# Performance work log

Measured on AMD Instinct MI355X. Metric: run time of the kernel, lower is better.

The kernel has to match this reference:

```python
import jax, jax.numpy as jnp
import numpy as np

N, E, F_IN, HID, OUT, HEADS, HC, L, EV, ED = 50000, 800000, 128, 96, 64, 8, 12, 6, 1000, 32
ACT_SLOPE = 0.01   # LeakyReLU default (act_layer)
ATT_SLOPE = 0.2    # GATv2 attention leaky relu
EPS = 1e-5         # GraphNorm eps


def setup_inputs() -> dict:
    key = jax.random.key(0)
    ks = jax.random.split(key, 16)
    r = lambda k, shp, s=0.05: jax.random.normal(k, shp, jnp.float32) * s
    z = lambda shp: jnp.zeros(shp, jnp.float32)
    o = lambda shp: jnp.ones(shp, jnp.float32)
    return {
        "x": jax.random.normal(ks[0], (N, F_IN), jnp.float32),
        "edge_index": jax.random.randint(ks[1], (2, E), 0, N),
        "edge_weight": jax.random.uniform(ks[2], (E,), jnp.float32),
        "edge_code": jax.random.randint(ks[3], (E,), 0, EV),
        "edge_emb": r(ks[4], (EV, ED), 0.1),
        "lin_in_W": r(ks[5], (F_IN, HID)), "lin_in_b": z((HID,)),
        "gn0_w": o((HID,)), "gn0_b": z((HID,)), "gn0_ms": o((HID,)),
        "Wl": r(ks[6], (L, HID, HID)), "bl": z((L, HID)),
        "Wr": r(ks[7], (L, HID, HID)), "br": z((L, HID)),
        "We": r(ks[8], (L, ED, HID)),
        "att": r(ks[9], (L, HEADS, HC)),
        "gbias": z((L, HID)),
        "gn_w": o((L, HID)), "gn_b": z((L, HID)), "gn_ms": o((L, HID)),
        "lin_out_W": r(ks[10], (HID, OUT)), "lin_out_b": z((OUT,)),
    }


def graph_norm(x, w, b, ms):
    # PyG GraphNorm on a single graph: mean over nodes, learnable mean scale
    mean = x.mean(axis=0, keepdims=True)
    out = x - ms * mean
    var = (out * out).mean(axis=0, keepdims=True)
    return w * out * jax.lax.rsqrt(var + EPS) + b


def gatv2_conv(h, src, dst, ew, ea, Wl_, bl_, Wr_, br_, We_, att_, bias_):
    # GATv2 with edge features; messages weighted by edge_weight (WGATv2Conv)
    xl = (h @ Wl_ + bl_).reshape(N, HEADS, HC)  # source transform
    xr = (h @ Wr_ + br_).reshape(N, HEADS, HC)  # target transform
    ee = (ea @ We_).reshape(E, HEADS, HC)       # edge transform
    s = jax.nn.leaky_relu(xl[src] + xr[dst] + ee, ATT_SLOPE)  # [E,H,C]
    logits = jnp.einsum('ehc,hc->eh', s, att_)  # [E,H]
    # numerically stable segment softmax over incoming edges of each dst node
    m = jax.ops.segment_max(logits, dst, num_segments=N)
    m = jnp.where(jnp.isfinite(m), m, 0.0)      # isolated nodes -> -inf max
    p = jnp.exp(logits - m[dst])
    zsum = jax.ops.segment_sum(p, dst, num_segments=N)
    alpha = p / (zsum[dst] + 1e-16)             # [E,H]
    msg = xl[src] * (alpha * ew[:, None])[..., None]  # [E,H,C]
    out = jax.ops.segment_sum(msg, dst, num_segments=N)  # [N,H,C]
    return out.reshape(N, HID) + bias_


def reference(x, edge_index, edge_weight, edge_code, edge_emb,
              lin_in_W, lin_in_b, gn0_w, gn0_b, gn0_ms,
              Wl, bl, Wr, br, We, att, gbias,
              gn_w, gn_b, gn_ms, lin_out_W, lin_out_b):
    src, dst = edge_index[0], edge_index[1]
    ea = edge_emb[edge_code]                    # [E,ED]
    h = graph_norm(x @ lin_in_W + lin_in_b, gn0_w, gn0_b, gn0_ms)
    for l in range(L):  # DeepGCNLayer 'res+': norm -> act -> conv, + residual
        t = graph_norm(h, gn_w[l], gn_b[l], gn_ms[l])
        t = jax.nn.leaky_relu(t, ACT_SLOPE)
        t = gatv2_conv(t, src, dst, edge_weight, ea,
                       Wl[l], bl[l], Wr[l], br[l], We[l], att[l], gbias[l])
        h = h + t
    return h @ lin_out_W + lin_out_b
```

## Files before the change

kernel.cpp:

```cpp
#include <hip/hip_runtime.h>
#include <hip/hip_bf16.h>

constexpr int NN   = 50000;
constexpr int NE   = 800000;
constexpr int FIN  = 128;
constexpr int HIDC = 96;
constexpr int FOUT = 64;
constexpr int NHEAD= 8;
constexpr int HCH  = 12;
constexpr int NLAY = 6;
constexpr int EVOC = 1000;
constexpr int EDIM = 32;
constexpr float ACT_SLOPE = 0.01f;
constexpr float ATT_SLOPE = 0.2f;
constexpr float GN_EPS = 1e-5f;
constexpr int GN_BLOCKS = 256;
constexpr int NSCB = (NN + 255)/256;

typedef __hip_bfloat16 bf16;
typedef __attribute__((ext_vector_type(8))) short bf16x8;
typedef __attribute__((ext_vector_type(4))) float f32x4;

__device__ __forceinline__ float bfu(unsigned u, int hi){
    return __uint_as_float(hi ? (u & 0xffff0000u) : (u << 16));
}

__global__ void k_hist(const int* __restrict__ dst, int* __restrict__ deg){
    int e = blockIdx.x*blockDim.x + threadIdx.x;
    if(e < NE) atomicAdd(&deg[dst[e]], 1);
}

__global__ __launch_bounds__(256) void k_scan1(const int* __restrict__ deg,
        int* __restrict__ pre, int* __restrict__ bsum){
    __shared__ int s[256];
    int tid = threadIdx.x;
    int idx = blockIdx.x*256 + tid;
    int v = (idx < NN) ? deg[idx] : 0;
    s[tid] = v; __syncthreads();
    #pragma unroll
    for(int off=1; off<256; off<<=1){
        int t = (tid>=off) ? s[tid-off] : 0;
        __syncthreads();
        s[tid] += t;
        __syncthreads();
    }
    if(idx < NN) pre[idx] = s[tid] - v;
    if(tid == 255) bsum[blockIdx.x] = s[255];
}

__global__ __launch_bounds__(256) void k_scan2(const int* __restrict__ bsum,
        int* __restrict__ boffs){
    __shared__ int s[256];
    int tid = threadIdx.x;
    int v = (tid < NSCB) ? bsum[tid] : 0;
    s[tid] = v; __syncthreads();
    #pragma unroll
    for(int off=1; off<256; off<<=1){
        int t = (tid>=off) ? s[tid-off] : 0;
        __syncthreads();
        s[tid] += t;
        __syncthreads();
    }
    if(tid < NSCB) boffs[tid] = s[tid] - v;
}

__global__ __launch_bounds__(256) void k_scan3(const int* __restrict__ pre,
        const int* __restrict__ boffs, int* __restrict__ rowptr, int* __restrict__ cursor){
    int tid = threadIdx.x;
    int idx = blockIdx.x*256 + tid;
    if(idx < NN){
        rowptr[idx] = pre[idx] + boffs[blockIdx.x];
        cursor[idx] = 0;
    }
    if(blockIdx.x == 0 && tid == 0) rowptr[NN] = NE;
}

__global__ void k_scatter(const int* __restrict__ src, const int* __restrict__ dst,
                          const int* __restrict__ code, const float* __restrict__ ew,
                          const int* __restrict__ rowptr, int* __restrict__ cursor,
                          int4* __restrict__ epk){
    int e = blockIdx.x*blockDim.x + threadIdx.x;
    if(e >= NE) return;
    int d = dst[e];
    int pos = rowptr[d] + atomicAdd(&cursor[d], 1);
    epk[pos] = make_int4(src[e], code[e], __float_as_int(ew[e]), 0);
}

__global__ __launch_bounds__(256) void k_trall(const float* __restrict__ Wl,
        const float* __restrict__ Wr, const float* __restrict__ Win, const float* __restrict__ Wout,
        bf16* __restrict__ wlt, bf16* __restrict__ wrt, bf16* __restrict__ wint, bf16* __restrict__ wot){
    int seg = blockIdx.y;
    const float* W; bf16* Wt; int K, N;
    if(seg < 6)      { W = Wl  + seg*9216;     Wt = wlt + seg*9216;     K = 96;  N = 96; }
    else if(seg < 12){ W = Wr  + (seg-6)*9216; Wt = wrt + (seg-6)*9216; K = 96;  N = 96; }
    else if(seg==12) { W = Win;                Wt = wint;               K = 128; N = 96; }
    else             { W = Wout;               Wt = wot;                K = 96;  N = 64; }
    int i = blockIdx.x*256 + threadIdx.x;
    if(i >= K*N) return;
    int k = i / N, nn = i - k*N;
    Wt[(size_t)nn*K + k] = __float2bfloat16(W[i]);
}

template<int K, int NC, typename OT>
__global__ __launch_bounds__(256) void k_gemm(const float* __restrict__ A,
        const float* __restrict__ W, const float* __restrict__ bias,
        OT* __restrict__ C, int M, int wstride, int cstride){
    constexpr int CPT = NC/16;
    W += (size_t)blockIdx.y * wstride;
    C += (size_t)blockIdx.y * cstride;
    __shared__ float At[K][68];
    int tid = threadIdx.x;
    int m0 = blockIdx.x*64;
    for(int i=tid; i<64*K; i+=256){
        int r = i / K, k = i - r*K;
        int row = m0 + r;
        At[k][r] = (row < M) ? A[(size_t)row*K + k] : 0.f;
    }
    __syncthreads();
    int tr = tid>>4, tc = tid&15;
    const float* wr = W + tc*CPT;
    float acc[4][CPT];
    #pragma unroll
    for(int i=0;i<4;i++)
        #pragma unroll
        for(int j=0;j<CPT;j++) acc[i][j]=0.f;
    #pragma unroll 4
    for(int k=0;k<K;k++){
        float a[4], w[CPT];
        #pragma unroll
        for(int i=0;i<4;i++) a[i] = At[k][tr*4+i];
        #pragma unroll
        for(int j=0;j<CPT;j++) w[j] = wr[k*NC + j];
        #pragma unroll
        for(int i=0;i<4;i++)
            #pragma unroll
            for(int j=0;j<CPT;j++) acc[i][j] += a[i]*w[j];
    }
    #pragma unroll
    for(int i=0;i<4;i++){
        int row = m0 + tr*4 + i;
        if(row < M){
            OT* cp = C + (size_t)row*NC + tc*CPT;
            #pragma unroll
            for(int j=0;j<CPT;j++){
                float v = acc[i][j] + (bias ? bias[tc*CPT+j] : 0.f);
                if constexpr (sizeof(OT)==2) cp[j] = __float2bfloat16(v);
                else cp[j] = v;
            }
        }
    }
}

template<int K, int NC, bool GN, bool DUAL, typename OT>
__global__ __launch_bounds__(256) void k_mfgemm(const float* __restrict__ A,
        const bf16* __restrict__ W1t, const float* __restrict__ b1,
        const bf16* __restrict__ W2t, const float* __restrict__ b2,
        const float* __restrict__ gscale, const float* __restrict__ gshift, float slope,
        OT* __restrict__ C1, OT* __restrict__ C2, int M){
    constexpr int KP = K + 8;
    constexpr int F4R = K/4;
    constexpr int NF4 = 64*F4R;
    constexpr int KS = K/32;
    constexpr int NT = NC/16;
    __shared__ bf16 At[64][KP];
    int tid = threadIdx.x;
    int m0 = blockIdx.x*64;
    for(int idx = tid; idx < NF4; idx += 256){
        int r = idx / F4R, c4 = idx - r*F4R;
        int row = m0 + r;
        float4 v = (row < M) ? ((const float4*)A)[(size_t)row*F4R + c4]
                             : make_float4(0.f,0.f,0.f,0.f);
        float vv[4] = {v.x, v.y, v.z, v.w};
        bf16* dp = &At[r][c4*4];
        #pragma unroll
        for(int c=0;c<4;c++){
            float u = vv[c];
            if constexpr (GN){
                int k = c4*4 + c;
                u = gscale[k]*u + gshift[k];
                u = (u > 0.f) ? u : slope*u;
            }
            dp[c] = __float2bfloat16(u);
        }
    }
    __syncthreads();
    int w = tid >> 6, l = tid & 63;
    int mrow = l & 15;
    int kg = (l >> 4) * 8;
    f32x4 acc1[NT], acc2[NT];
    #pragma unroll
    for(int nt=0; nt<NT; nt++){
        acc1[nt] = (f32x4){0.f,0.f,0.f,0.f};
        if constexpr (DUAL) acc2[nt] = (f32x4){0.f,0.f,0.f,0.f};
    }
    const bf16* a_base = &At[w*16 + mrow][0];
    #pragma unroll
    for(int ks=0; ks<KS; ks++){
        bf16x8 a = *(const bf16x8*)(a_base + ks*32 + kg);
        #pragma unroll
        for(int nt=0; nt<NT; nt++){
            int n = nt*16 + mrow;
            bf16x8 bfr = *(const bf16x8*)(W1t + (size_t)n*K + ks*32 + kg);
            acc1[nt] = __builtin_amdgcn_mfma_f32_16x16x32_bf16(a, bfr, acc1[nt], 0,0,0);
            if constexpr (DUAL){
                bf16x8 bfr2 = *(const bf16x8*)(W2t + (size_t)n*K + ks*32 + kg);
                acc2[nt] = __builtin_amdgcn_mfma_f32_16x16x32_bf16(a, bfr2, acc2[nt], 0,0,0);
            }
        }
    }
    int rbase = m0 + w*16 + (l>>4)*4;
    #pragma unroll
    for(int nt=0; nt<NT; nt++){
        int n = nt*16 + mrow;
        float bb1 = b1[n];
        float bb2 = 0.f;
        if constexpr (DUAL) bb2 = b2[n];
        #pragma unroll
        for(int r=0;r<4;r++){
            int row = rbase + r;
            if(row < M){
                float v1 = acc1[nt][r] + bb1;
                if constexpr (sizeof(OT)==2) C1[(size_t)row*NC + n] = __float2bfloat16(v1);
                else                         C1[(size_t)row*NC + n] = v1;
                if constexpr (DUAL){
                    float v2 = acc2[nt][r] + bb2;
                    C2[(size_t)row*NC + n] = __float2bfloat16(v2);
                }
            }
        }
    }
}

__global__ __launch_bounds__(384) void k_gn_reduce(const float* __restrict__ x, float* __restrict__ partial){
    int tid = threadIdx.x;
    const float4* x4 = (const float4*)x;
    constexpr int TOT4 = NN*HIDC/4;
    const int stride = GN_BLOCKS*384;
    float s0=0,s1=0,s2=0,s3=0, q0=0,q1=0,q2=0,q3=0;
    for(int i = blockIdx.x*384 + tid; i < TOT4; i += stride){
        float4 v = x4[i];
        s0+=v.x; q0+=v.x*v.x;
        s1+=v.y; q1+=v.y*v.y;
        s2+=v.z; q2+=v.z*v.z;
        s3+=v.w; q3+=v.w*v.w;
    }
    __shared__ float ls[384][4], lq[384][4];
    ls[tid][0]=s0; ls[tid][1]=s1; ls[tid][2]=s2; ls[tid][3]=s3;
    lq[tid][0]=q0; lq[tid][1]=q1; lq[tid][2]=q2; lq[tid][3]=q3;
    __syncthreads();
    if(tid < 96){
        int g = tid >> 2, c = tid & 3;
        float a=0.f, b=0.f;
        #pragma unroll
        for(int j=0;j<16;j++){
            a += ls[g + 24*j][c];
            b += lq[g + 24*j][c];
        }
        partial[blockIdx.x*192 + g*4 + c]      = a;
        partial[blockIdx.x*192 + 96 + g*4 + c] = b;
    }
}

__global__ __launch_bounds__(768) void k_gn_finalize(const float* __restrict__ partial,
        const float* __restrict__ w, const float* __restrict__ b, const float* __restrict__ ms,
        float* __restrict__ scale, float* __restrict__ shift){
    __shared__ float red[4][192];
    int tid = threadIdx.x;
    int v = tid % 192, seg = tid / 192;
    float s = 0.f;
    #pragma unroll 8
    for(int bk=seg; bk<GN_BLOCKS; bk+=4) s += partial[bk*192 + v];
    red[seg][v] = s;
    __syncthreads();
    if(tid < 192) red[0][tid] = red[0][tid]+red[1][tid]+red[2][tid]+red[3][tid];
    __syncthreads();
    if(tid < HIDC){
        float mean = red[0][tid] / (float)NN;
        float m2   = red[0][tid+96] / (float)NN;
        float mm   = ms[tid]*mean;
        float var  = m2 - 2.f*mm*mean + mm*mm;
        float sc   = w[tid] * rsqrtf(var + GN_EPS);
        scale[tid] = sc;
        shift[tid] = b[tid] - sc*mm;
    }
}

__global__ __launch_bounds__(384) void k_gn_apply(const float* __restrict__ x,
        const float* __restrict__ scale, const float* __restrict__ shift,
        float* __restrict__ out, float slope){
    int tid = threadIdx.x;
    int c = tid % HIDC;
    float sc = scale[c], sh = shift[c];
    const int total = NN*HIDC;
    const int stride = gridDim.x*384;
    for(int i=blockIdx.x*384+tid; i<total; i+=stride){
        float v = sc*x[i] + sh;
        out[i] = (v > 0.f) ? v : slope*v;
    }
}

__global__ __launch_bounds__(256, 6) void k_gat(const int* __restrict__ rowptr,
        const int4* __restrict__ epk,
        const bf16* __restrict__ xl, const bf16* __restrict__ xr,
        const bf16* __restrict__ eW, const float* __restrict__ att_l,
        const float* __restrict__ gbias_l, float* __restrict__ h){
    int wid  = threadIdx.x >> 6;
    int lane = threadIdx.x & 63;
    int n = blockIdx.x*4 + wid;
    if(n >= NN) return;
    int r0 = rowptr[n], r1 = rowptr[n+1];
    int e_loc = lane >> 3, hh = lane & 7;
    float xrv[HCH], atv[HCH];
    {
        const uint2* x2 = (const uint2*)(xr + (size_t)n*HIDC + hh*HCH);
        #pragma unroll
        for(int q=0;q<3;q++){
            uint2 u = x2[q];
            xrv[q*4+0]=bfu(u.x,0); xrv[q*4+1]=bfu(u.x,1);
            xrv[q*4+2]=bfu(u.y,0); xrv[q*4+3]=bfu(u.y,1);
        }
        const float4* a4 = (const float4*)(att_l + hh*HCH);
        #pragma unroll
        for(int q=0;q<3;q++){
            float4 f = a4[q];
            atv[q*4+0]=f.x; atv[q*4+1]=f.y; atv[q*4+2]=f.z; atv[q*4+3]=f.w;
        }
    }
    float m = -3.0e38f, z = 0.f;
    float acc[HCH];
    #pragma unroll
    for(int q=0;q<HCH;q++) acc[q]=0.f;
    for(int base = r0; base < r1; base += 8){
        int eidx = base + e_loc;
        bool val = eidx < r1;
        float xv[HCH];
        float lg = -3.0e38f, ew = 0.f;
        if(val){
            int4 ec = epk[eidx];
            ew = __int_as_float(ec.z);
            const uint2* xa2 = (const uint2*)(xl + (size_t)ec.x*HIDC + hh*HCH);
            const uint2* eb2 = (const uint2*)(eW + (size_t)ec.y*HIDC + hh*HCH);
            uint2 xa[3] = {xa2[0], xa2[1], xa2[2]};
            uint2 eb[3] = {eb2[0], eb2[1], eb2[2]};
            float dot = 0.f;
            #pragma unroll
            for(int q=0;q<3;q++){
                unsigned ux[2] = {xa[q].x, xa[q].y};
                unsigned ue[2] = {eb[q].x, eb[q].y};
                #pragma unroll
                for(int k2=0;k2<4;k2++){
                    int c = q*4 + k2;
                    float xf = bfu(ux[k2>>1], k2&1);
                    xv[c] = xf;
                    float v = xf + xrv[c] + bfu(ue[k2>>1], k2&1);
                    v = fmaxf(v, ATT_SLOPE*v);
                    dot += v * atv[c];
                }
            }
            lg = dot;
        } else {
            #pragma unroll
            for(int q=0;q<HCH;q++) xv[q]=0.f;
        }
        float tm = lg;
        tm = fmaxf(tm, __shfl_xor(tm, 8));
        tm = fmaxf(tm, __shfl_xor(tm, 16));
        tm = fmaxf(tm, __shfl_xor(tm, 32));
        float mn = fmaxf(m, tm);
        float sc = __expf(m - mn);
        float p  = __expf(lg - mn);
        float zt = p;
        zt += __shfl_xor(zt, 8); zt += __shfl_xor(zt, 16); zt += __shfl_xor(zt, 32);
        z = z*sc + zt;
        m = mn;
        float pw = p * ew;
        #pragma unroll
        for(int q=0;q<HCH;q++) acc[q] = acc[q]*sc + pw*xv[q];
    }
    #pragma unroll
    for(int q=0;q<HCH;q++){
        float a = acc[q];
        a += __shfl_xor(a, 8);
        a += __shfl_xor(a, 16);
        a += __shfl_xor(a, 32);
        acc[q] = a;
    }
    if(e_loc == 0){
        float inv = 1.f/(z + 1e-16f);
        float4* hp4 = (float4*)(h + (size_t)n*HIDC + hh*HCH);
        const float4* gb4 = (const float4*)(gbias_l + hh*HCH);
        #pragma unroll
        for(int q3=0;q3<3;q3++){
            float4 hv = hp4[q3], gv = gb4[q3];
            hv.x += acc[q3*4+0]*inv + gv.x;
            hv.y += acc[q3*4+1]*inv + gv.y;
            hv.z += acc[q3*4+2]*inv + gv.z;
            hv.w += acc[q3*4+3]*inv + gv.w;
            hp4[q3] = hv;
        }
    }
}

extern "C" void kernel_launch(void* const* d_in, const int* in_sizes, int n_in,
                              void* d_out, int out_size, void* d_ws, size_t ws_size,
                              hipStream_t stream) {
    (void)in_sizes; (void)n_in; (void)out_size; (void)ws_size;
    const float* x          = (const float*)d_in[0];
    const int*   edge_index = (const int*)  d_in[1];
    const float* edge_weight= (const float*)d_in[2];
    const int*   edge_code  = (const int*)  d_in[3];
    const float* edge_emb   = (const float*)d_in[4];
    const float* lin_in_W   = (const float*)d_in[5];
    const float* lin_in_b   = (const float*)d_in[6];
    const float* gn0_w      = (const float*)d_in[7];
    const float* gn0_b      = (const float*)d_in[8];
    const float* gn0_ms     = (const float*)d_in[9];
    const float* Wl         = (const float*)d_in[10];
    const float* bl         = (const float*)d_in[11];
    const float* Wr         = (const float*)d_in[12];
    const float* br         = (const float*)d_in[13];
    const float* We         = (const float*)d_in[14];
    const float* att        = (const float*)d_in[15];
    const float* gbias      = (const float*)d_in[16];
    const float* gn_w       = (const float*)d_in[17];
    const float* gn_b       = (const float*)d_in[18];
    const float* gn_ms      = (const float*)d_in[19];
    const float* lin_out_W  = (const float*)d_in[20];
    const float* lin_out_b  = (const float*)d_in[21];
    float* out = (float*)d_out;

    char* ws = (char*)d_ws;
    size_t off = 0;
    auto alloc = [&](size_t bytes)->void*{ void* p = ws + off; off += (bytes + 255) & ~(size_t)255; return p; };
    float* h     = (float*)alloc((size_t)NN*HIDC*4);
    bf16*  xl    = (bf16*) alloc((size_t)NN*HIDC*2);
    bf16*  xr    = (bf16*) alloc((size_t)NN*HIDC*2);
    bf16*  eWa   = (bf16*) alloc((size_t)NLAY*EVOC*HIDC*2);
    bf16*  wlt   = (bf16*) alloc((size_t)NLAY*HIDC*HIDC*2);
    bf16*  wrt   = (bf16*) alloc((size_t)NLAY*HIDC*HIDC*2);
    bf16*  wint  = (bf16*) alloc((size_t)FIN*HIDC*2);
    bf16*  wot   = (bf16*) alloc((size_t)HIDC*FOUT*2);
    float* partial=(float*)alloc((size_t)GN_BLOCKS*2*HIDC*4);
    float* scale = (float*)alloc(HIDC*4);
    float* shift = (float*)alloc(HIDC*4);
    int* rowptr  = (int*)alloc((size_t)(NN+1)*4);
    int* cursor  = (int*)alloc((size_t)NN*4);
    int* pre     = (int*)alloc((size_t)NN*4);
    int* bsum    = (int*)alloc((size_t)NSCB*4);
    int* boffs   = (int*)alloc((size_t)NSCB*4);
    int4* epk    = (int4*)alloc((size_t)NE*16);

    const int* src = edge_index;
    const int* dst = edge_index + NE;

    hipMemsetAsync(cursor, 0, (size_t)NN*4, stream);
    k_hist<<<(NE+255)/256, 256, 0, stream>>>(dst, cursor);
    k_scan1<<<NSCB, 256, 0, stream>>>(cursor, pre, bsum);
    k_scan2<<<1, 256, 0, stream>>>(bsum, boffs);
    k_scan3<<<NSCB, 256, 0, stream>>>(pre, boffs, rowptr, cursor);
    k_scatter<<<(NE+255)/256, 256, 0, stream>>>(src, dst, edge_code, edge_weight,
                                                rowptr, cursor, epk);

    k_trall<<<dim3(48, 14), 256, 0, stream>>>(Wl, Wr, lin_in_W, lin_out_W,
                                              wlt, wrt, wint, wot);

    k_gemm<EDIM,HIDC,bf16><<<dim3((EVOC+63)/64, NLAY), 256, 0, stream>>>(
        edge_emb, We, nullptr, eWa, EVOC, EDIM*HIDC, EVOC*HIDC);

    k_mfgemm<FIN,HIDC,false,false,float><<<(NN+63)/64, 256, 0, stream>>>(
        x, wint, lin_in_b, nullptr, nullptr, nullptr, nullptr, 0.f, h, nullptr, NN);

    k_gn_reduce<<<GN_BLOCKS, 384, 0, stream>>>(h, partial);
    k_gn_finalize<<<1, 768, 0, stream>>>(partial, gn0_w, gn0_b, gn0_ms, scale, shift);
    k_gn_apply<<<768, 384, 0, stream>>>(h, scale, shift, h, 1.0f);

    for(int l=0;l<NLAY;l++){
        k_gn_reduce<<<GN_BLOCKS, 384, 0, stream>>>(h, partial);
        k_gn_finalize<<<1, 768, 0, stream>>>(partial, gn_w + l*HIDC, gn_b + l*HIDC, gn_ms + l*HIDC, scale, shift);
        k_mfgemm<HIDC,HIDC,true,true,bf16><<<(NN+63)/64, 256, 0, stream>>>(
            h, wlt + (size_t)l*HIDC*HIDC, bl + l*HIDC,
               wrt + (size_t)l*HIDC*HIDC, br + l*HIDC,
            scale, shift, ACT_SLOPE, xl, xr, NN);
        k_gat<<<(NN+3)/4, 256, 0, stream>>>(rowptr, epk, xl, xr,
                                            eWa + (size_t)l*EVOC*HIDC, att + l*NHEAD*HCH,
                                            gbias + l*HIDC, h);
    }

    k_mfgemm<HIDC,FOUT,false,false,float><<<(NN+63)/64, 256, 0, stream>>>(
        h, wot, lin_out_b, nullptr, nullptr, nullptr, nullptr, 0.f, out, nullptr, NN);
}
```

Measured before the change: 660.6 us.

## Switch GAT path to packed fp16, shrink edge records, fuse GraphNorm finalize

Moves intermediate features, weights and edge embeddings from bf16 to fp16. The GAT kernel now does its attention math and message accumulation in packed half2 arithmetic with fdot2, instead of unpacking to fp32. Edge records shrink from 16 to 8 bytes by packing source index and edge code into one 32-bit word. The GraphNorm finalize step is folded into the reduce kernel through a last-block atomic counter, which removes a launch per norm. The risks are precision loss from accumulating the softmax-weighted sum in fp16 and possible overflow, since fp16 has a narrower range than bf16.

```diff
diff --git a/kernel.cpp b/kernel.cpp
--- a/kernel.cpp
+++ b/kernel.cpp
@@ -17,12 +17,26 @@
 constexpr int GN_BLOCKS = 256;
 constexpr int NSCB = (NN + 255)/256;
 
-typedef __hip_bfloat16 bf16;
-typedef __attribute__((ext_vector_type(8))) short bf16x8;
+typedef _Float16 f16;
+typedef __attribute__((ext_vector_type(2))) _Float16 h2;
+typedef __attribute__((ext_vector_type(8))) _Float16 f16x8;
 typedef __attribute__((ext_vector_type(4))) float f32x4;
 
-__device__ __forceinline__ float bfu(unsigned u, int hi){
-    return __uint_as_float(hi ? (u & 0xffff0000u) : (u << 16));
+__device__ __forceinline__ h2 bch2(unsigned u){ return __builtin_bit_cast(h2, u); }
+__device__ __forceinline__ unsigned bcu(h2 v){ return __builtin_bit_cast(unsigned, v); }
+
+__device__ __forceinline__ float dot2(h2 a, h2 b, float c){
+#if __has_builtin(__builtin_amdgcn_fdot2)
+    return __builtin_amdgcn_fdot2(a, b, c, false);
+#else
+    return c + (float)a.x*(float)b.x + (float)a.y*(float)b.y;
+#endif
+}
+
+template<typename OT>
+__device__ __forceinline__ OT cvt_out(float v){
+    if constexpr (sizeof(OT)==2) return (OT)v;
+    else return v;
 }
 
 __global__ void k_hist(const int* __restrict__ dst, int* __restrict__ deg){
@@ -78,19 +92,20 @@
 __global__ void k_scatter(const int* __restrict__ src, const int* __restrict__ dst,
                           const int* __restrict__ code, const float* __restrict__ ew,
                           const int* __restrict__ rowptr, int* __restrict__ cursor,
-                          int4* __restrict__ epk){
+                          int2* __restrict__ epk){
     int e = blockIdx.x*blockDim.x + threadIdx.x;
     if(e >= NE) return;
     int d = dst[e];
     int pos = rowptr[d] + atomicAdd(&cursor[d], 1);
-    epk[pos] = make_int4(src[e], code[e], __float_as_int(ew[e]), 0);
+    epk[pos] = make_int2((int)(((unsigned)code[e] << 16) | (unsigned)src[e]),
+                         __float_as_int(ew[e]));
 }
 
 __global__ __launch_bounds__(256) void k_trall(const float* __restrict__ Wl,
         const float* __restrict__ Wr, const float* __restrict__ Win, const float* __restrict__ Wout,
-        bf16* __restrict__ wlt, bf16* __restrict__ wrt, bf16* __restrict__ wint, bf16* __restrict__ wot){
+        f16* __restrict__ wlt, f16* __restrict__ wrt, f16* __restrict__ wint, f16* __restrict__ wot){
     int seg = blockIdx.y;
-    const float* W; bf16* Wt; int K, N;
+    const float* W; f16* Wt; int K, N;
     if(seg < 6)      { W = Wl  + seg*9216;     Wt = wlt + seg*9216;     K = 96;  N = 96; }
     else if(seg < 12){ W = Wr  + (seg-6)*9216; Wt = wrt + (seg-6)*9216; K = 96;  N = 96; }
     else if(seg==12) { W = Win;                Wt = wint;               K = 128; N = 96; }
@@ -98,7 +113,7 @@
     int i = blockIdx.x*256 + threadIdx.x;
     if(i >= K*N) return;
     int k = i / N, nn = i - k*N;
-    Wt[(size_t)nn*K + k] = __float2bfloat16(W[i]);
+    Wt[(size_t)nn*K + k] = (f16)W[i];
 }
 
 template<int K, int NC, typename OT>
@@ -144,8 +159,7 @@
             #pragma unroll
             for(int j=0;j<CPT;j++){
                 float v = acc[i][j] + (bias ? bias[tc*CPT+j] : 0.f);
-                if constexpr (sizeof(OT)==2) cp[j] = __float2bfloat16(v);
-                else cp[j] = v;
+                cp[j] = cvt_out<OT>(v);
             }
         }
     }
@@ -153,8 +167,8 @@
 
 template<int K, int NC, bool GN, bool DUAL, typename OT>
 __global__ __launch_bounds__(256) void k_mfgemm(const float* __restrict__ A,
-        const bf16* __restrict__ W1t, const float* __restrict__ b1,
-        const bf16* __restrict__ W2t, const float* __restrict__ b2,
+        const f16* __restrict__ W1t, const float* __restrict__ b1,
+        const f16* __restrict__ W2t, const float* __restrict__ b2,
         const float* __restrict__ gscale, const float* __restrict__ gshift, float slope,
         OT* __restrict__ C1, OT* __restrict__ C2, int M){
     constexpr int KP = K + 8;
@@ -162,7 +176,7 @@
     constexpr int NF4 = 64*F4R;
     constexpr int KS = K/32;
     constexpr int NT = NC/16;
-    __shared__ bf16 At[64][KP];
+    __shared__ f16 At[64][KP];
     int tid = threadIdx.x;
     int m0 = blockIdx.x*64;
     for(int idx = tid; idx < NF4; idx += 256){
@@ -171,7 +185,7 @@
         float4 v = (row < M) ? ((const float4*)A)[(size_t)row*F4R + c4]
                              : make_float4(0.f,0.f,0.f,0.f);
         float vv[4] = {v.x, v.y, v.z, v.w};
-        bf16* dp = &At[r][c4*4];
+        f16* dp = &At[r][c4*4];
         #pragma unroll
         for(int c=0;c<4;c++){
             float u = vv[c];
@@ -180,7 +194,7 @@
                 u = gscale[k]*u + gshift[k];
                 u = (u > 0.f) ? u : slope*u;
             }
-            dp[c] = __float2bfloat16(u);
+            dp[c] = (f16)u;
         }
     }
     __syncthreads();
@@ -193,18 +207,18 @@
         acc1[nt] = (f32x4){0.f,0.f,0.f,0.f};
         if constexpr (DUAL) acc2[nt] = (f32x4){0.f,0.f,0.f,0.f};
     }
-    const bf16* a_base = &At[w*16 + mrow][0];
+    const f16* a_base = &At[w*16 + mrow][0];
     #pragma unroll
     for(int ks=0; ks<KS; ks++){
-        bf16x8 a = *(const bf16x8*)(a_base + ks*32 + kg);
+        f16x8 a = *(const f16x8*)(a_base + ks*32 + kg);
         #pragma unroll
         for(int nt=0; nt<NT; nt++){
             int n = nt*16 + mrow;
-            bf16x8 bfr = *(const bf16x8*)(W1t + (size_t)n*K + ks*32 + kg);
-            acc1[nt] = __builtin_amdgcn_mfma_f32_16x16x32_bf16(a, bfr, acc1[nt], 0,0,0);
+            f16x8 bfr = *(const f16x8*)(W1t + (size_t)n*K + ks*32 + kg);
+            acc1[nt] = __builtin_amdgcn_mfma_f32_16x16x32_f16(a, bfr, acc1[nt], 0,0,0);
             if constexpr (DUAL){
-                bf16x8 bfr2 = *(const bf16x8*)(W2t + (size_t)n*K + ks*32 + kg);
-                acc2[nt] = __builtin_amdgcn_mfma_f32_16x16x32_bf16(a, bfr2, acc2[nt], 0,0,0);
+                f16x8 bfr2 = *(const f16x8*)(W2t + (size_t)n*K + ks*32 + kg);
+                acc2[nt] = __builtin_amdgcn_mfma_f32_16x16x32_f16(a, bfr2, acc2[nt], 0,0,0);
             }
         }
     }
@@ -219,19 +233,18 @@
         for(int r=0;r<4;r++){
             int row = rbase + r;
             if(row < M){
-                float v1 = acc1[nt][r] + bb1;
-                if constexpr (sizeof(OT)==2) C1[(size_t)row*NC + n] = __float2bfloat16(v1);
-                else                         C1[(size_t)row*NC + n] = v1;
-                if constexpr (DUAL){
-                    float v2 = acc2[nt][r] + bb2;
-                    C2[(size_t)row*NC + n] = __float2bfloat16(v2);
-                }
+                C1[(size_t)row*NC + n] = cvt_out<OT>(acc1[nt][r] + bb1);
+                if constexpr (DUAL)
+                    C2[(size_t)row*NC + n] = cvt_out<OT>(acc2[nt][r] + bb2);
             }
         }
     }
 }
 
-__global__ __launch_bounds__(384) void k_gn_reduce(const float* __restrict__ x, float* __restrict__ partial){
+__global__ __launch_bounds__(384) void k_gn_reduce(const float* __restrict__ x,
+        float* __restrict__ partial, int* __restrict__ counter,
+        const float* __restrict__ w, const float* __restrict__ b, const float* __restrict__ ms,
+        float* __restrict__ scale, float* __restrict__ shift){
     int tid = threadIdx.x;
     const float4* x4 = (const float4*)x;
     constexpr int TOT4 = NN*HIDC/4;
@@ -250,29 +263,30 @@
     __syncthreads();
     if(tid < 96){
         int g = tid >> 2, c = tid & 3;
-        float a=0.f, b=0.f;
+        float a=0.f, bq=0.f;
         #pragma unroll
         for(int j=0;j<16;j++){
-            a += ls[g + 24*j][c];
-            b += lq[g + 24*j][c];
+            a  += ls[g + 24*j][c];
+            bq += lq[g + 24*j][c];
         }
         partial[blockIdx.x*192 + g*4 + c]      = a;
-        partial[blockIdx.x*192 + 96 + g*4 + c] = b;
-    }
-}
-
-__global__ __launch_bounds__(768) void k_gn_finalize(const float* __restrict__ partial,
-        const float* __restrict__ w, const float* __restrict__ b, const float* __restrict__ ms,
-        float* __restrict__ scale, float* __restrict__ shift){
-    __shared__ float red[4][192];
-    int tid = threadIdx.x;
+        partial[blockIdx.x*192 + 96 + g*4 + c] = bq;
+    }
+    __syncthreads();
+    __threadfence();
+    __shared__ int isLast;
+    if(tid == 0) isLast = (atomicAdd(counter, 1) == GN_BLOCKS-1);
+    __syncthreads();
+    if(!isLast) return;
+    __threadfence();
+    __shared__ float red[2][192];
     int v = tid % 192, seg = tid / 192;
     float s = 0.f;
     #pragma unroll 8
-    for(int bk=seg; bk<GN_BLOCKS; bk+=4) s += partial[bk*192 + v];
+    for(int bk=seg; bk<GN_BLOCKS; bk+=2) s += partial[bk*192 + v];
     red[seg][v] = s;
     __syncthreads();
-    if(tid < 192) red[0][tid] = red[0][tid]+red[1][tid]+red[2][tid]+red[3][tid];
+    if(tid < 192) red[0][tid] += red[1][tid];
     __syncthreads();
     if(tid < HIDC){
         float mean = red[0][tid] / (float)NN;
@@ -299,10 +313,10 @@
     }
 }
 
-__global__ __launch_bounds__(256, 6) void k_gat(const int* __restrict__ rowptr,
-        const int4* __restrict__ epk,
-        const bf16* __restrict__ xl, const bf16* __restrict__ xr,
-        const bf16* __restrict__ eW, const float* __restrict__ att_l,
+__global__ __launch_bounds__(256, 8) void k_gat(const int* __restrict__ rowptr,
+        const int2* __restrict__ epk,
+        const f16* __restrict__ xl, const f16* __restrict__ xr,
+        const f16* __restrict__ eW, const float* __restrict__ att_l,
         const float* __restrict__ gbias_l, float* __restrict__ h){
     int wid  = threadIdx.x >> 6;
     int lane = threadIdx.x & 63;
@@ -310,57 +324,58 @@
     if(n >= NN) return;
     int r0 = rowptr[n], r1 = rowptr[n+1];
     int e_loc = lane >> 3, hh = lane & 7;
-    float xrv[HCH], atv[HCH];
+    h2 xrh[6], ath[6];
     {
         const uint2* x2 = (const uint2*)(xr + (size_t)n*HIDC + hh*HCH);
         #pragma unroll
         for(int q=0;q<3;q++){
             uint2 u = x2[q];
-            xrv[q*4+0]=bfu(u.x,0); xrv[q*4+1]=bfu(u.x,1);
-            xrv[q*4+2]=bfu(u.y,0); xrv[q*4+3]=bfu(u.y,1);
-        }
-        const float4* a4 = (const float4*)(att_l + hh*HCH);
-        #pragma unroll
-        for(int q=0;q<3;q++){
-            float4 f = a4[q];
-            atv[q*4+0]=f.x; atv[q*4+1]=f.y; atv[q*4+2]=f.z; atv[q*4+3]=f.w;
-        }
-    }
+            xrh[2*q] = bch2(u.x); xrh[2*q+1] = bch2(u.y);
+        }
+        const float2* a2 = (const float2*)(att_l + hh*HCH);
+        #pragma unroll
+        for(int q=0;q<6;q++){
+            float2 f = a2[q];
+            ath[q] = (h2){(f16)f.x, (f16)f.y};
+        }
+    }
+    const h2 slope2 = (h2){(f16)ATT_SLOPE, (f16)ATT_SLOPE};
     float m = -3.0e38f, z = 0.f;
-    float acc[HCH];
-    #pragma unroll
-    for(int q=0;q<HCH;q++) acc[q]=0.f;
+    h2 acc[6];
+    #pragma unroll
+    for(int q=0;q<6;q++) acc[q] = (h2){(f16)0, (f16)0};
     for(int base = r0; base < r1; base += 8){
         int eidx = base + e_loc;
         bool val = eidx < r1;
-        float xv[HCH];
+        h2 xa[6];
         float lg = -3.0e38f, ew = 0.f;
         if(val){
-            int4 ec = epk[eidx];
-            ew = __int_as_float(ec.z);
-            const uint2* xa2 = (const uint2*)(xl + (size_t)ec.x*HIDC + hh*HCH);
-            const uint2* eb2 = (const uint2*)(eW + (size_t)ec.y*HIDC + hh*HCH);
-            uint2 xa[3] = {xa2[0], xa2[1], xa2[2]};
-            uint2 eb[3] = {eb2[0], eb2[1], eb2[2]};
+            int2 ec = epk[eidx];
+            unsigned sc_pack = (unsigned)ec.x;
+            int s  = sc_pack & 0xffffu;
+            int cd = sc_pack >> 16;
+            ew = __int_as_float(ec.y);
+            const uint2* xa2 = (const uint2*)(xl + (size_t)s*HIDC + hh*HCH);
+            const uint2* eb2 = (const uint2*)(eW + (size_t)cd*HIDC + hh*HCH);
+            uint2 xraw[3] = {xa2[0], xa2[1], xa2[2]};
+            uint2 eraw[3] = {eb2[0], eb2[1], eb2[2]};
             float dot = 0.f;
             #pragma unroll
             for(int q=0;q<3;q++){
-                unsigned ux[2] = {xa[q].x, xa[q].y};
-                unsigned ue[2] = {eb[q].x, eb[q].y};
-                #pragma unroll
-                for(int k2=0;k2<4;k2++){
-                    int c = q*4 + k2;
-                    float xf = bfu(ux[k2>>1], k2&1);
-                    xv[c] = xf;
-                    float v = xf + xrv[c] + bfu(ue[k2>>1], k2&1);
-                    v = fmaxf(v, ATT_SLOPE*v);
-                    dot += v * atv[c];
-                }
+                h2 x0 = bch2(xraw[q].x), x1 = bch2(xraw[q].y);
+                h2 e0 = bch2(eraw[q].x), e1 = bch2(eraw[q].y);
+                xa[2*q] = x0; xa[2*q+1] = x1;
+                h2 v0 = x0 + xrh[2*q]   + e0;
+                h2 v1 = x1 + xrh[2*q+1] + e1;
+                v0 = __builtin_elementwise_max(v0, v0*slope2);
+                v1 = __builtin_elementwise_max(v1, v1*slope2);
+                dot = dot2(v0, ath[2*q],   dot);
+                dot = dot2(v1, ath[2*q+1], dot);
             }
             lg = dot;
         } else {
             #pragma unroll
-            for(int q=0;q<HCH;q++) xv[q]=0.f;
+            for(int q=0;q<6;q++) xa[q] = (h2){(f16)0, (f16)0};
         }
         float tm = lg;
         tm = fmaxf(tm, __shfl_xor(tm, 8));
@@ -373,16 +388,19 @@
         zt += __shfl_xor(zt, 8); zt += __shfl_xor(zt, 16); zt += __shfl_xor(zt, 32);
         z = z*sc + zt;
         m = mn;
-        float pw = p * ew;
-        #pragma unroll
-        for(int q=0;q<HCH;q++) acc[q] = acc[q]*sc + pw*xv[q];
-    }
-    #pragma unroll
-    for(int q=0;q<HCH;q++){
-        float a = acc[q];
-        a += __shfl_xor(a, 8);
-        a += __shfl_xor(a, 16);
-        a += __shfl_xor(a, 32);
+        f16 pwh = (f16)(p * ew);
+        f16 sch = (f16)sc;
+        h2 pw2 = (h2){pwh, pwh};
+        h2 sc2 = (h2){sch, sch};
+        #pragma unroll
+        for(int q=0;q<6;q++) acc[q] = acc[q]*sc2 + pw2*xa[q];
+    }
+    #pragma unroll
+    for(int q=0;q<6;q++){
+        h2 a = acc[q];
+        a = a + bch2((unsigned)__shfl_xor((int)bcu(a), 8));
+        a = a + bch2((unsigned)__shfl_xor((int)bcu(a), 16));
+        a = a + bch2((unsigned)__shfl_xor((int)bcu(a), 32));
         acc[q] = a;
     }
     if(e_loc == 0){
@@ -392,10 +410,11 @@
         #pragma unroll
         for(int q3=0;q3<3;q3++){
             float4 hv = hp4[q3], gv = gb4[q3];
-            hv.x += acc[q3*4+0]*inv + gv.x;
-            hv.y += acc[q3*4+1]*inv + gv.y;
-            hv.z += acc[q3*4+2]*inv + gv.z;
-            hv.w += acc[q3*4+3]*inv + gv.w;
+            h2 a0 = acc[q3*2], a1 = acc[q3*2+1];
+            hv.x += (float)a0.x*inv + gv.x;
+            hv.y += (float)a0.y*inv + gv.y;
+            hv.z += (float)a1.x*inv + gv.z;
+            hv.w += (float)a1.y*inv + gv.w;
             hp4[q3] = hv;
         }
     }
@@ -433,27 +452,30 @@
     size_t off = 0;
     auto alloc = [&](size_t bytes)->void*{ void* p = ws + off; off += (bytes + 255) & ~(size_t)255; return p; };
     float* h     = (float*)alloc((size_t)NN*HIDC*4);
-    bf16*  xl    = (bf16*) alloc((size_t)NN*HIDC*2);
-    bf16*  xr    = (bf16*) alloc((size_t)NN*HIDC*2);
-    bf16*  eWa   = (bf16*) alloc((size_t)NLAY*EVOC*HIDC*2);
-    bf16*  wlt   = (bf16*) alloc((size_t)NLAY*HIDC*HIDC*2);
-    bf16*  wrt   = (bf16*) alloc((size_t)NLAY*HIDC*HIDC*2);
-    bf16*  wint  = (bf16*) alloc((size_t)FIN*HIDC*2);
-    bf16*  wot   = (bf16*) alloc((size_t)HIDC*FOUT*2);
+    f16*   xl    = (f16*)  alloc((size_t)NN*HIDC*2);
+    f16*   xr    = (f16*)  alloc((size_t)NN*HIDC*2);
+    f16*   eWa   = (f16*)  alloc((size_t)NLAY*EVOC*HIDC*2);
+    f16*   wlt   = (f16*)  alloc((size_t)NLAY*HIDC*HIDC*2);
+    f16*   wrt   = (f16*)  alloc((size_t)NLAY*HIDC*HIDC*2);
+    f16*   wint  = (f16*)  alloc((size_t)FIN*HIDC*2);
+    f16*   wot   = (f16*)  alloc((size_t)HIDC*FOUT*2);
     float* partial=(float*)alloc((size_t)GN_BLOCKS*2*HIDC*4);
     float* scale = (float*)alloc(HIDC*4);
     float* shift = (float*)alloc(HIDC*4);
+    int* gncnt   = (int*)alloc(8*4);
     int* rowptr  = (int*)alloc((size_t)(NN+1)*4);
     int* cursor  = (int*)alloc((size_t)NN*4);
     int* pre     = (int*)alloc((size_t)NN*4);
     int* bsum    = (int*)alloc((size_t)NSCB*4);
     int* boffs   = (int*)alloc((size_t)NSCB*4);
-    int4* epk    = (int4*)alloc((size_t)NE*16);
+    int2* epk    = (int2*)alloc((size_t)NE*8);
 
     const int* src = edge_index;
     const int* dst = edge_index + NE;
 
     hipMemsetAsync(cursor, 0, (size_t)NN*4, stream);
+    hipMemsetAsync(gncnt, 0, 8*4, stream);
+
     k_hist<<<(NE+255)/256, 256, 0, stream>>>(dst, cursor);
     k_scan1<<<NSCB, 256, 0, stream>>>(cursor, pre, bsum);
     k_scan2<<<1, 256, 0, stream>>>(bsum, boffs);
@@ -464,20 +486,21 @@
     k_trall<<<dim3(48, 14), 256, 0, stream>>>(Wl, Wr, lin_in_W, lin_out_W,
                                               wlt, wrt, wint, wot);
 
-    k_gemm<EDIM,HIDC,bf16><<<dim3((EVOC+63)/64, NLAY), 256, 0, stream>>>(
+    k_gemm<EDIM,HIDC,f16><<<dim3((EVOC+63)/64, NLAY), 256, 0, stream>>>(
         edge_emb, We, nullptr, eWa, EVOC, EDIM*HIDC, EVOC*HIDC);
 
     k_mfgemm<FIN,HIDC,false,false,float><<<(NN+63)/64, 256, 0, stream>>>(
         x, wint, lin_in_b, nullptr, nullptr, nullptr, nullptr, 0.f, h, nullptr, NN);
 
-    k_gn_reduce<<<GN_BLOCKS, 384, 0, stream>>>(h, partial);
-    k_gn_finalize<<<1, 768, 0, stream>>>(partial, gn0_w, gn0_b, gn0_ms, scale, shift);
+    k_gn_reduce<<<GN_BLOCKS, 384, 0, stream>>>(h, partial, gncnt+0,
+                                               gn0_w, gn0_b, gn0_ms, scale, shift);
     k_gn_apply<<<768, 384, 0, stream>>>(h, scale, shift, h, 1.0f);
 
     for(int l=0;l<NLAY;l++){
-        k_gn_reduce<<<GN_BLOCKS, 384, 0, stream>>>(h, partial);
-        k_gn_finalize<<<1, 768, 0, stream>>>(partial, gn_w + l*HIDC, gn_b + l*HIDC, gn_ms + l*HIDC, scale, shift);
-        k_mfgemm<HIDC,HIDC,true,true,bf16><<<(NN+63)/64, 256, 0, stream>>>(
+        k_gn_reduce<<<GN_BLOCKS, 384, 0, stream>>>(h, partial, gncnt+1+l,
+                                                   gn_w + l*HIDC, gn_b + l*HIDC, gn_ms + l*HIDC,
+                                                   scale, shift);
+        k_mfgemm<HIDC,HIDC,true,true,f16><<<(NN+63)/64, 256, 0, stream>>>(
             h, wlt + (size_t)l*HIDC*HIDC, bl + l*HIDC,
                wrt + (size_t)l*HIDC*HIDC, br + l*HIDC,
             scale, shift, ACT_SLOPE, xl, xr, NN);
```

Measured after the change: 778.2 us. 1.18x slower.
